# Performance work log

Hardware: AMD Instinct MI355X
Metric: run time of the kernel (lower is better)

## Reference

```python
import jax, jax.numpy as jnp
import numpy as np

E = 8
D_IN = 1024
D_HID = 4096
D_OUT = 1024
T = 16384  # total tokens, equally split: 2048 per expert


def setup_inputs() -> dict:
    key = jax.random.key(0)
    k1, k2, k3, k4, k5 = jax.random.split(key, 5)
    x = jax.random.normal(k1, (T, D_IN), dtype=jnp.float32)
    cnt = jnp.full((E,), T // E, dtype=jnp.int32)  # tokens per expert (sorted/contiguous)
    s1 = 1.0 / np.sqrt(D_IN)
    s2 = 1.0 / np.sqrt(D_HID)
    w1 = jax.random.uniform(k2, (E, D_HID, D_IN), jnp.float32, -s1, s1)
    b1 = jax.random.uniform(k3, (E, D_HID), jnp.float32, -s1, s1)
    w2 = jax.random.uniform(k4, (E, D_OUT, D_HID), jnp.float32, -s2, s2)
    b2 = jax.random.uniform(k5, (E, D_OUT), jnp.float32, -s2, s2)
    return {"x": x, "cnt": cnt, "w1": w1, "b1": b1, "w2": w2, "b2": b2}


def reference(x, cnt, w1, b1, w2, b2):
    # FMoELinear: tokens are laid out contiguously by expert per `cnt`.
    # With equal counts (T // E per expert) the grouped GEMM is a batched einsum.
    e = w1.shape[0]
    t, d = x.shape
    cap = t // e  # tokens per expert
    xg = x.reshape(e, cap, d)                               # [E, cap, d_in]
    h = jnp.einsum('ecd,ehd->ech', xg, w1) + b1[:, None, :]  # fc1: [E, cap, d_hid]
    h = jax.nn.gelu(h, approximate=False)                    # nn.GELU (exact erf)
    # drop1 / drop2 are p=0.0 (identity); sub_norm is Identity (use_subln=False)
    y = jnp.einsum('ech,eoh->eco', h, w2) + b2[:, None, :]   # fc2: [E, cap, d_out]
    return y.reshape(t, -1)
```

## Files before the change

kernel.cpp:

```cpp
#include <hip/hip_runtime.h>
#include <hip/hip_bf16.h>
#include <cstdint>

#define NUM_E 8
#define DIN   1024
#define DHID  4096
#define DOUTP 1024
#define TTOK  16384
#define CAP   2048

typedef __attribute__((ext_vector_type(8))) short bf16x8;
typedef __attribute__((ext_vector_type(4))) float f32x4;

static __device__ __forceinline__ ushort f32_to_bf16_rne(float f) {
  uint32_t b = __float_as_uint(f);
  b += 0x7fffu + ((b >> 16) & 1u);
  return (ushort)(b >> 16);
}

__global__ void __launch_bounds__(256) cvt_bf16_kernel(const float* __restrict__ in,
                                                       ushort* __restrict__ out,
                                                       unsigned n) {
  unsigned i = (blockIdx.x * 256u + threadIdx.x) * 8u;
  const unsigned stride = gridDim.x * 256u * 8u;
  for (; i < n; i += stride) {
    float4 a = *reinterpret_cast<const float4*>(in + i);
    float4 b = *reinterpret_cast<const float4*>(in + i + 4);
    union { ushort u[8]; uint4 v; } o;
    o.u[0] = f32_to_bf16_rne(a.x); o.u[1] = f32_to_bf16_rne(a.y);
    o.u[2] = f32_to_bf16_rne(a.z); o.u[3] = f32_to_bf16_rne(a.w);
    o.u[4] = f32_to_bf16_rne(b.x); o.u[5] = f32_to_bf16_rne(b.y);
    o.u[6] = f32_to_bf16_rne(b.z); o.u[7] = f32_to_bf16_rne(b.w);
    *reinterpret_cast<uint4*>(out + i) = o.v;
  }
}

#define GLD(g, l)                                                                 \
  __builtin_amdgcn_global_load_lds((const __attribute__((address_space(1))) void*)(g), \
                                   (__attribute__((address_space(3))) void*)(l), 16, 0, 0)

template <int K, int N, int TILES_N, bool GELU_BF16_OUT>
__global__ void __launch_bounds__(512, 1) grouped_gemm_kernel(
    const ushort* __restrict__ A,
    const ushort* __restrict__ B,
    const float* __restrict__ bias,
    void* __restrict__ Cout) {
  constexpr int TILES_M = CAP / 256;
  constexpr int BPE = TILES_M * TILES_N;
  constexpr int NT = K / 64;
  static_assert(NT >= 4, "pipeline needs >=4 K-tiles");

  __shared__ uint8_t lds[131072];

  const int tid = (blockIdx.x & 7) * BPE + (blockIdx.x >> 3);
  const int e   = tid / BPE;
  const int rm  = tid % BPE;
  const int nt  = rm / TILES_M;
  const int mt  = rm % TILES_M;

  const int t  = threadIdx.x;
  const int w  = t >> 6, l = t & 63;
  const int wm = w >> 2, wn = w & 3;
  const int lr = l & 15;
  const int kg = l >> 4;
  const int col0 = nt * 256 + wn * 64;

  const int gr  = t >> 3;
  const int sch = (t & 7) ^ (gr & 7);
  const ushort* gA = A + ((long)(e * CAP + mt * 256) + gr) * K + sch * 8;
  const ushort* gB = B + ((long)(e * N) + nt * 256 + gr) * K + sch * 8;
  uint8_t* const dT = lds + t * 16;

#define SA(j, h) { const ushort* s_ = gA + (long)(h) * 128 * K + (long)(j) * 64;   \
    uint8_t* d_ = dT + (((j) & 1) << 16) + ((h) << 14);                            \
    GLD(s_, d_); GLD(s_ + (long)64 * K, d_ + 8192); }
#define SB(j, h) { const ushort* s_ = gB + (long)(h) * 128 * K + (long)(j) * 64;   \
    uint8_t* d_ = dT + (((j) & 1) << 16) + 32768 + ((h) << 14);                    \
    GLD(s_, d_); GLD(s_ + (long)64 * K, d_ + 8192); }

  int offA[8][2], offB[4][2];
#pragma unroll
  for (int m = 0; m < 8; ++m) {
    const int r = m * 16 + lr;
#pragma unroll
    for (int kh = 0; kh < 2; ++kh)
      offA[m][kh] = r * 128 + ((((kh << 2) | kg) ^ (r & 7)) << 4);
  }
#pragma unroll
  for (int n = 0; n < 4; ++n) {
    const int r = (wn & 1) * 64 + n * 16 + lr;
#pragma unroll
    for (int kh = 0; kh < 2; ++kh)
      offB[n][kh] = r * 128 + ((((kh << 2) | kg) ^ (r & 7)) << 4);
  }
  const int rdAoff = wm << 14;
  const int rdBoff = 32768 + ((wn >> 1) << 14);

  f32x4 acc[8][4] = {};

  SA(0, 0); SA(0, 1); SB(0, 0); SB(0, 1);
  SB(1, 0); SB(1, 1); SA(1, 0);
  asm volatile("s_waitcnt vmcnt(6)" ::: "memory");
  __builtin_amdgcn_s_barrier();

  for (int T = 0; T < NT; ++T) {
    const uint8_t* rdA = lds + ((T & 1) << 16) + rdAoff;
    const uint8_t* rdB = lds + ((T & 1) << 16) + rdBoff;
    bf16x8 a0[4][2], a1[4][2], b0[2][2], b1[2][2];

#pragma unroll
    for (int m = 0; m < 4; ++m)
#pragma unroll
      for (int kh = 0; kh < 2; ++kh)
        a0[m][kh] = *reinterpret_cast<const bf16x8*>(rdA + offA[m][kh]);
#pragma unroll
    for (int n = 0; n < 2; ++n)
#pragma unroll
      for (int kh = 0; kh < 2; ++kh)
        b0[n][kh] = *reinterpret_cast<const bf16x8*>(rdB + offB[n][kh]);
    if (T + 1 < NT) SA(T + 1, 1);
    __builtin_amdgcn_s_barrier();
    asm volatile("s_waitcnt lgkmcnt(0)" ::: "memory");
    __builtin_amdgcn_sched_barrier(0);
    __builtin_amdgcn_s_setprio(1);
#pragma unroll
    for (int m = 0; m < 4; ++m)
#pragma unroll
      for (int n = 0; n < 2; ++n)
#pragma unroll
        for (int kh = 0; kh < 2; ++kh)
          acc[m][n] = __builtin_amdgcn_mfma_f32_16x16x32_bf16(a0[m][kh], b0[n][kh], acc[m][n], 0, 0, 0);
    __builtin_amdgcn_s_setprio(0);
    __builtin_amdgcn_s_barrier();

#pragma unroll
    for (int n = 0; n < 2; ++n)
#pragma unroll
      for (int kh = 0; kh < 2; ++kh)
        b1[n][kh] = *reinterpret_cast<const bf16x8*>(rdB + offB[n + 2][kh]);
    __builtin_amdgcn_s_barrier();
    asm volatile("s_waitcnt lgkmcnt(0)" ::: "memory");
    __builtin_amdgcn_sched_barrier(0);
    __builtin_amdgcn_s_setprio(1);
#pragma unroll
    for (int m = 0; m < 4; ++m)
#pragma unroll
      for (int n = 0; n < 2; ++n)
#pragma unroll
        for (int kh = 0; kh < 2; ++kh)
          acc[m][n + 2] = __builtin_amdgcn_mfma_f32_16x16x32_bf16(a0[m][kh], b1[n][kh], acc[m][n + 2], 0, 0, 0);
    __builtin_amdgcn_s_setprio(0);
    __builtin_amdgcn_s_barrier();

#pragma unroll
    for (int m = 0; m < 4; ++m)
#pragma unroll
      for (int kh = 0; kh < 2; ++kh)
        a1[m][kh] = *reinterpret_cast<const bf16x8*>(rdA + offA[m + 4][kh]);
    if (T + 2 < NT) SB(T + 2, 0);
    __builtin_amdgcn_s_barrier();
    asm volatile("s_waitcnt lgkmcnt(0)" ::: "memory");
    __builtin_amdgcn_sched_barrier(0);
    __builtin_amdgcn_s_setprio(1);
#pragma unroll
    for (int m = 0; m < 4; ++m)
#pragma unroll
      for (int n = 0; n < 2; ++n)
#pragma unroll
        for (int kh = 0; kh < 2; ++kh)
          acc[m + 4][n + 2] = __builtin_amdgcn_mfma_f32_16x16x32_bf16(a1[m][kh], b1[n][kh], acc[m + 4][n + 2], 0, 0, 0);
    __builtin_amdgcn_s_setprio(0);
    __builtin_amdgcn_s_barrier();

    if (T + 2 < NT) { SB(T + 2, 1); SA(T + 2, 0); }
    __builtin_amdgcn_s_barrier();
    asm volatile("s_waitcnt lgkmcnt(0)" ::: "memory");
    __builtin_amdgcn_sched_barrier(0);
    __builtin_amdgcn_s_setprio(1);
#pragma unroll
    for (int m = 0; m < 4; ++m)
#pragma unroll
      for (int n = 0; n < 2; ++n)
#pragma unroll
        for (int kh = 0; kh < 2; ++kh)
          acc[m + 4][n] = __builtin_amdgcn_mfma_f32_16x16x32_bf16(a1[m][kh], b0[n][kh], acc[m + 4][n], 0, 0, 0);
    __builtin_amdgcn_s_setprio(0);
    if (T < NT - 2) {
      asm volatile("s_waitcnt vmcnt(6)" ::: "memory");
    } else if (T == NT - 2) {
      asm volatile("s_waitcnt vmcnt(0)" ::: "memory");
    }
    __builtin_amdgcn_s_barrier();
  }

  const long rowg0 = (long)e * CAP + mt * 256 + wm * 128;
  float bv[4];
#pragma unroll
  for (int n = 0; n < 4; ++n) bv[n] = bias[(long)e * N + col0 + n * 16 + lr];

  if constexpr (GELU_BF16_OUT) {
    uint8_t* const sl = lds + (w << 14);
#pragma unroll
    for (int n = 0; n < 4; ++n) {
#pragma unroll
      for (int m = 0; m < 8; ++m) {
#pragma unroll
        for (int q = 0; q < 4; ++q) {
          const int r = m * 16 + kg * 4 + q;
          const int c = n * 16 + lr;
          float v = acc[m][n][q] + bv[n];
          v = 0.5f * v * (1.0f + erff(v * 0.70710678118654752f));
          *(ushort*)(sl + r * 128 + ((((c >> 3) ^ (r & 7))) << 4) + (c & 7) * 2) =
              f32_to_bf16_rne(v);
        }
      }
    }
    asm volatile("s_waitcnt lgkmcnt(0)" ::: "memory");
    ushort* const Cb = (ushort*)Cout;
#pragma unroll
    for (int it = 0; it < 16; ++it) {
      const int idx = it * 64 + l;
      const int r = idx >> 3, c16 = idx & 7;
      uint4 vv = *reinterpret_cast<const uint4*>(sl + r * 128 + ((c16 ^ (r & 7)) << 4));
      *reinterpret_cast<uint4*>(Cb + (rowg0 + r) * N + col0 + c16 * 8) = vv;
    }
  } else {
    float* const Cf = (float*)Cout;
#pragma unroll
    for (int n = 0; n < 4; ++n) {
#pragma unroll
      for (int m = 0; m < 8; ++m) {
#pragma unroll
        for (int q = 0; q < 4; ++q) {
          const int r = m * 16 + kg * 4 + q;
          Cf[(rowg0 + r) * N + col0 + n * 16 + lr] = acc[m][n][q] + bv[n];
        }
      }
    }
  }
#undef SA
#undef SB
}

extern "C" void kernel_launch(void* const* d_in, const int* in_sizes, int n_in,
                              void* d_out, int out_size, void* d_ws, size_t ws_size,
                              hipStream_t stream) {
  const float* x  = (const float*)d_in[0];
  const float* w1 = (const float*)d_in[2];
  const float* b1 = (const float*)d_in[3];
  const float* w2 = (const float*)d_in[4];
  const float* b2 = (const float*)d_in[5];
  float* out = (float*)d_out;

  constexpr size_t W2B_OFF = 67108864;
  constexpr size_t HB_OFF  = 134217728;
  constexpr size_t WS_NEED = 268435456;
  if (ws_size < WS_NEED) return;

  ushort* w1b = (ushort*)d_ws;
  ushort* w2b = (ushort*)d_ws + W2B_OFF;
  ushort* hb  = (ushort*)d_ws + HB_OFF;
  ushort* xb  = (ushort*)d_out;

  cvt_bf16_kernel<<<2048, 256, 0, stream>>>(x,  xb,  (unsigned)(TTOK * DIN));
  cvt_bf16_kernel<<<2048, 256, 0, stream>>>(w1, w1b, (unsigned)(NUM_E * DHID * DIN));
  cvt_bf16_kernel<<<2048, 256, 0, stream>>>(w2, w2b, (unsigned)(NUM_E * DOUTP * DHID));

  grouped_gemm_kernel<DIN, DHID, DHID / 256, true>
      <<<dim3(NUM_E * (CAP / 256) * (DHID / 256)), 512, 0, stream>>>(xb, w1b, b1, hb);

  grouped_gemm_kernel<DHID, DOUTP, DOUTP / 256, false>
      <<<dim3(NUM_E * (CAP / 256) * (DOUTP / 256)), 512, 0, stream>>>(hb, w2b, b2, out);
}
```

Measured before the change: 409.6 us.

## Unroll GEMM main loop by two with shifted prefetch schedule and fast erf

The K-loop is unrolled by two so each LDS buffer address is a compile-time constant, and the global-to-LDS prefetches are redistributed: A tiles for the next step load earlier while B loads two steps ahead, with adjusted vmcnt waits. The GELU epilogue replaces erff with an Abramowitz-Stegun polynomial approximation using rcp and expf. This aims to cut address arithmetic and smooth memory/MFMA overlap, and to make the epilogue cheaper. The risks are a subtle ordering bug in the new prefetch and wait scheme, and a small loss of accuracy from the approximate erf (~1e-7 abs error, under bf16 precision).

Measured after the change: 375.5 us. 8.3% less time.

```diff
diff --git a/kernel.cpp b/kernel.cpp
--- a/kernel.cpp
+++ b/kernel.cpp
@@ -16,6 +16,19 @@
   uint32_t b = __float_as_uint(f);
   b += 0x7fffu + ((b >> 16) & 1u);
   return (ushort)(b >> 16);
+}
+
+static __device__ __forceinline__ float erf_fast(float x) {
+  const float ax = __builtin_fabsf(x);
+  const float t  = __builtin_amdgcn_rcpf(__builtin_fmaf(0.3275911f, ax, 1.0f));
+  float p = __builtin_fmaf(1.061405429f, t, -1.453152027f);
+  p = __builtin_fmaf(p, t, 1.421413741f);
+  p = __builtin_fmaf(p, t, -0.284496736f);
+  p = __builtin_fmaf(p, t, 0.254829592f);
+  p = p * t;
+  const float e = __expf(-ax * ax);
+  const float r = __builtin_fmaf(-p, e, 1.0f);
+  return __builtin_copysignf(r, x);
 }
 
 __global__ void __launch_bounds__(256) cvt_bf16_kernel(const float* __restrict__ in,
@@ -48,7 +61,8 @@
   constexpr int TILES_M = CAP / 256;
   constexpr int BPE = TILES_M * TILES_N;
   constexpr int NT = K / 64;
-  static_assert(NT >= 4, "pipeline needs >=4 K-tiles");
+  constexpr int NTI = NT / 2;
+  static_assert(NT >= 4 && (NT & 1) == 0, "need even NT >= 4");
 
   __shared__ uint8_t lds[131072];
 
@@ -99,97 +113,90 @@
   f32x4 acc[8][4] = {};
 
   SA(0, 0); SA(0, 1); SB(0, 0); SB(0, 1);
-  SB(1, 0); SB(1, 1); SA(1, 0);
-  asm volatile("s_waitcnt vmcnt(6)" ::: "memory");
+  SB(1, 0); SB(1, 1);
+  asm volatile("s_waitcnt vmcnt(4)" ::: "memory");
   __builtin_amdgcn_s_barrier();
 
-  for (int T = 0; T < NT; ++T) {
-    const uint8_t* rdA = lds + ((T & 1) << 16) + rdAoff;
-    const uint8_t* rdB = lds + ((T & 1) << 16) + rdBoff;
+#define PHASE_MFMA(AF, BF, AI, NI)                                                 \
+    __builtin_amdgcn_s_barrier();                                                  \
+    asm volatile("s_waitcnt lgkmcnt(0)" ::: "memory");                             \
+    __builtin_amdgcn_sched_barrier(0);                                             \
+    __builtin_amdgcn_s_setprio(1);                                                 \
+    _Pragma("unroll")                                                              \
+    for (int m = 0; m < 4; ++m)                                                    \
+      _Pragma("unroll")                                                            \
+      for (int n = 0; n < 2; ++n)                                                  \
+        _Pragma("unroll")                                                          \
+        for (int kh = 0; kh < 2; ++kh)                                             \
+          acc[m + (AI)][n + (NI)] = __builtin_amdgcn_mfma_f32_16x16x32_bf16(       \
+              AF[m][kh], BF[n][kh], acc[m + (AI)][n + (NI)], 0, 0, 0);             \
+    __builtin_amdgcn_s_setprio(0);
+
+#define RD_A0(SRC) _Pragma("unroll")                                               \
+    for (int m = 0; m < 4; ++m) _Pragma("unroll")                                  \
+      for (int kh = 0; kh < 2; ++kh)                                               \
+        a0[m][kh] = *reinterpret_cast<const bf16x8*>((SRC) + offA[m][kh]);
+#define RD_A1(SRC) _Pragma("unroll")                                               \
+    for (int m = 0; m < 4; ++m) _Pragma("unroll")                                  \
+      for (int kh = 0; kh < 2; ++kh)                                               \
+        a1[m][kh] = *reinterpret_cast<const bf16x8*>((SRC) + offA[m + 4][kh]);
+#define RD_B0(SRC) _Pragma("unroll")                                               \
+    for (int n = 0; n < 2; ++n) _Pragma("unroll")                                  \
+      for (int kh = 0; kh < 2; ++kh)                                               \
+        b0[n][kh] = *reinterpret_cast<const bf16x8*>((SRC) + offB[n][kh]);
+#define RD_B1(SRC) _Pragma("unroll")                                               \
+    for (int n = 0; n < 2; ++n) _Pragma("unroll")                                  \
+      for (int kh = 0; kh < 2; ++kh)                                               \
+        b1[n][kh] = *reinterpret_cast<const bf16x8*>((SRC) + offB[n + 2][kh]);
+
+  for (int i = 0; i < NTI; ++i) {
+    const int u = 2 * i, v = u + 1;
+    const bool st = (u + 2) < NT;
+    const uint8_t* rA0 = lds + rdAoff;
+    const uint8_t* rB0 = lds + rdBoff;
+    const uint8_t* rA1 = lds + 65536 + rdAoff;
+    const uint8_t* rB1 = lds + 65536 + rdBoff;
     bf16x8 a0[4][2], a1[4][2], b0[2][2], b1[2][2];
 
-#pragma unroll
-    for (int m = 0; m < 4; ++m)
-#pragma unroll
-      for (int kh = 0; kh < 2; ++kh)
-        a0[m][kh] = *reinterpret_cast<const bf16x8*>(rdA + offA[m][kh]);
-#pragma unroll
-    for (int n = 0; n < 2; ++n)
-#pragma unroll
-      for (int kh = 0; kh < 2; ++kh)
-        b0[n][kh] = *reinterpret_cast<const bf16x8*>(rdB + offB[n][kh]);
-    if (T + 1 < NT) SA(T + 1, 1);
-    __builtin_amdgcn_s_barrier();
-    asm volatile("s_waitcnt lgkmcnt(0)" ::: "memory");
-    __builtin_amdgcn_sched_barrier(0);
-    __builtin_amdgcn_s_setprio(1);
-#pragma unroll
-    for (int m = 0; m < 4; ++m)
-#pragma unroll
-      for (int n = 0; n < 2; ++n)
-#pragma unroll
-        for (int kh = 0; kh < 2; ++kh)
-          acc[m][n] = __builtin_amdgcn_mfma_f32_16x16x32_bf16(a0[m][kh], b0[n][kh], acc[m][n], 0, 0, 0);
-    __builtin_amdgcn_s_setprio(0);
-    __builtin_amdgcn_s_barrier();
-
-#pragma unroll
-    for (int n = 0; n < 2; ++n)
-#pragma unroll
-      for (int kh = 0; kh < 2; ++kh)
-        b1[n][kh] = *reinterpret_cast<const bf16x8*>(rdB + offB[n + 2][kh]);
-    __builtin_amdgcn_s_barrier();
-    asm volatile("s_waitcnt lgkmcnt(0)" ::: "memory");
-    __builtin_amdgcn_sched_barrier(0);
-    __builtin_amdgcn_s_setprio(1);
-#pragma unroll
-    for (int m = 0; m < 4; ++m)
-#pragma unroll
-      for (int n = 0; n < 2; ++n)
-#pragma unroll
-        for (int kh = 0; kh < 2; ++kh)
-          acc[m][n + 2] = __builtin_amdgcn_mfma_f32_16x16x32_bf16(a0[m][kh], b1[n][kh], acc[m][n + 2], 0, 0, 0);
-    __builtin_amdgcn_s_setprio(0);
-    __builtin_amdgcn_s_barrier();
-
-#pragma unroll
-    for (int m = 0; m < 4; ++m)
-#pragma unroll
-      for (int kh = 0; kh < 2; ++kh)
-        a1[m][kh] = *reinterpret_cast<const bf16x8*>(rdA + offA[m + 4][kh]);
-    if (T + 2 < NT) SB(T + 2, 0);
-    __builtin_amdgcn_s_barrier();
-    asm volatile("s_waitcnt lgkmcnt(0)" ::: "memory");
-    __builtin_amdgcn_sched_barrier(0);
-    __builtin_amdgcn_s_setprio(1);
-#pragma unroll
-    for (int m = 0; m < 4; ++m)
-#pragma unroll
-      for (int n = 0; n < 2; ++n)
-#pragma unroll
-        for (int kh = 0; kh < 2; ++kh)
-          acc[m + 4][n + 2] = __builtin_amdgcn_mfma_f32_16x16x32_bf16(a1[m][kh], b1[n][kh], acc[m + 4][n + 2], 0, 0, 0);
-    __builtin_amdgcn_s_setprio(0);
-    __builtin_amdgcn_s_barrier();
-
-    if (T + 2 < NT) { SB(T + 2, 1); SA(T + 2, 0); }
-    __builtin_amdgcn_s_barrier();
-    asm volatile("s_waitcnt lgkmcnt(0)" ::: "memory");
-    __builtin_amdgcn_sched_barrier(0);
-    __builtin_amdgcn_s_setprio(1);
-#pragma unroll
-    for (int m = 0; m < 4; ++m)
-#pragma unroll
-      for (int n = 0; n < 2; ++n)
-#pragma unroll
-        for (int kh = 0; kh < 2; ++kh)
-          acc[m + 4][n] = __builtin_amdgcn_mfma_f32_16x16x32_bf16(a1[m][kh], b0[n][kh], acc[m + 4][n], 0, 0, 0);
-    __builtin_amdgcn_s_setprio(0);
-    if (T < NT - 2) {
-      asm volatile("s_waitcnt vmcnt(6)" ::: "memory");
-    } else if (T == NT - 2) {
-      asm volatile("s_waitcnt vmcnt(0)" ::: "memory");
-    }
+    RD_A0(rA0) RD_B0(rB0)
+    SA(v, 0);
+    PHASE_MFMA(a0, b0, 0, 0)
+    __builtin_amdgcn_s_barrier();
+
+    RD_B1(rB0)
+    SA(v, 1);
+    PHASE_MFMA(a0, b1, 0, 2)
+    __builtin_amdgcn_s_barrier();
+
+    RD_A1(rA0)
+    if (st) SB(u + 2, 0);
+    PHASE_MFMA(a1, b1, 4, 2)
+    __builtin_amdgcn_s_barrier();
+
+    if (st) SB(u + 2, 1);
+    PHASE_MFMA(a1, b0, 4, 0)
+    if (st) { asm volatile("s_waitcnt vmcnt(4)" ::: "memory"); }
+    else    { asm volatile("s_waitcnt vmcnt(0)" ::: "memory"); }
+    __builtin_amdgcn_s_barrier();
+
+    RD_A0(rA1) RD_B0(rB1)
+    if (st) SA(u + 2, 0);
+    PHASE_MFMA(a0, b0, 0, 0)
+    __builtin_amdgcn_s_barrier();
+
+    RD_B1(rB1)
+    if (st) SA(u + 2, 1);
+    PHASE_MFMA(a0, b1, 0, 2)
+    __builtin_amdgcn_s_barrier();
+
+    RD_A1(rA1)
+    if (st) SB(v + 2, 0);
+    PHASE_MFMA(a1, b1, 4, 2)
+    __builtin_amdgcn_s_barrier();
+
+    if (st) SB(v + 2, 1);
+    PHASE_MFMA(a1, b0, 4, 0)
+    if (st) { asm volatile("s_waitcnt vmcnt(4)" ::: "memory"); }
     __builtin_amdgcn_s_barrier();
   }
 
@@ -208,10 +215,10 @@
         for (int q = 0; q < 4; ++q) {
           const int r = m * 16 + kg * 4 + q;
           const int c = n * 16 + lr;
-          float v = acc[m][n][q] + bv[n];
-          v = 0.5f * v * (1.0f + erff(v * 0.70710678118654752f));
+          float vx = acc[m][n][q] + bv[n];
+          vx = 0.5f * vx * (1.0f + erf_fast(vx * 0.70710678118654752f));
           *(ushort*)(sl + r * 128 + ((((c >> 3) ^ (r & 7))) << 4) + (c & 7) * 2) =
-              f32_to_bf16_rne(v);
+              f32_to_bf16_rne(vx);
         }
       }
     }
@@ -240,6 +247,11 @@
   }
 #undef SA
 #undef SB
+#undef PHASE_MFMA
+#undef RD_A0
+#undef RD_A1
+#undef RD_B0
+#undef RD_B1
 }
 
 extern "C" void kernel_launch(void* const* d_in, const int* in_sizes, int n_in,
```
